# Optimization experiments

Measured on AMD Instinct MI355X. Metric: run time of the kernel, lower is better.

Reference implementation:

```python
import jax, jax.numpy as jnp
import numpy as np

# PyG ChebConv defaults: normalization='sym', lambda_max=2.0.
# L_hat = 2*L/lambda_max - I = (I - D^-1/2 A D^-1/2) - I = -D^-1/2 A D^-1/2
# (self-loop/diagonal coefficient is exactly 0 when lambda_max == 2).

N_NODES = 30000
IN_CH = 128
HID_CH = 256
K = 3
N_EDGES = 480000


def _norm_weights(edge_index, n):
    src, dst = edge_index[0], edge_index[1]
    mask = src != dst  # remove_self_loops
    ones = jnp.where(mask, 1.0, 0.0)
    deg = jax.ops.segment_sum(ones, src, num_segments=n)
    dis = jnp.where(deg > 0, deg ** -0.5, 0.0)  # deg_inv_sqrt, inf -> 0
    w = jnp.where(mask, -dis[src] * dis[dst], 0.0)  # -A_sym edge weights
    return src, dst, w


def _cheb_conv(x, src, dst, w, W, b, n):
    # Tx_0 = x; Tx_1 = L_hat x; Tx_k = 2 L_hat Tx_{k-1} - Tx_{k-2}
    def lap(h):  # sparse matvec: (L_hat h)[i] = sum_{e: dst_e=i} w_e * h[src_e]
        return jax.ops.segment_sum(w[:, None] * h[src], dst, num_segments=n)

    Tx_prev = x
    out = x @ W[0]
    if W.shape[0] > 1:
        Tx_cur = lap(x)
        out = out + Tx_cur @ W[1]
        for k in range(2, W.shape[0]):
            Tx_next = 2.0 * lap(Tx_cur) - Tx_prev
            out = out + Tx_next @ W[k]
            Tx_prev, Tx_cur = Tx_cur, Tx_next
    return out + b


def setup_inputs() -> dict:
    key = jax.random.key(0)
    k1, k2, k3, k4, k5, k6 = jax.random.split(key, 6)
    x = jax.random.normal(k1, (N_NODES, IN_CH), dtype=jnp.float32)
    edge_index = jax.random.randint(k2, (2, N_EDGES), 0, N_NODES, dtype=jnp.int64)
    s1 = (1.0 / (IN_CH * K)) ** 0.5
    s2 = (1.0 / (HID_CH * K)) ** 0.5
    W1 = jax.random.uniform(k3, (K, IN_CH, HID_CH), jnp.float32, -s1, s1)
    b1 = jax.random.uniform(k4, (HID_CH,), jnp.float32, -s1, s1)
    W2 = jax.random.uniform(k5, (K, HID_CH, IN_CH), jnp.float32, -s2, s2)
    b2 = jax.random.uniform(k6, (IN_CH,), jnp.float32, -s2, s2)
    return {"x": x, "edge_index": edge_index, "W1": W1, "b1": b1, "W2": W2, "b2": b2}


def reference(x, edge_index, W1, b1, W2, b2):
    n = x.shape[0]
    src, dst, w = _norm_weights(edge_index, n)
    h = jax.nn.relu(_cheb_conv(x, src, dst, w, W1, b1, n))
    return _cheb_conv(h, src, dst, w, W2, b2, n)
```

## Files before the change

kernel.cpp:

```cpp
#include <hip/hip_runtime.h>
#include <hip/hip_bf16.h>


#define ELLW 64

typedef short bf16x8_t __attribute__((ext_vector_type(8)));
typedef unsigned short u16x4_t __attribute__((ext_vector_type(4)));
typedef unsigned short u16x8_t __attribute__((ext_vector_type(8)));
typedef float f32x4_t __attribute__((ext_vector_type(4)));

static __device__ inline unsigned short f2bf(float f) {
    __hip_bfloat16 h = __float2bfloat16(f);
    return __builtin_bit_cast(unsigned short, h);
}
static __device__ inline float bfbits2f(unsigned int lo16) {
    unsigned int u = lo16 << 16;
    return __builtin_bit_cast(float, u);
}

__global__ __launch_bounds__(256) void build_kernel(const int* __restrict__ src,
                                                    const int* __restrict__ dst,
                                                    int* __restrict__ degi,
                                                    int* __restrict__ cnt,
                                                    unsigned short* __restrict__ ell,
                                                    int E) {
    int e = blockIdx.x * 256 + threadIdx.x;
    if (e >= E) return;
    int s = src[e], d = dst[e];
    if (s != d) atomicAdd(&degi[s], 1);
    int pos = atomicAdd(&cnt[d], 1);
    if (pos < ELLW) ell[(size_t)d * ELLW + pos] = (unsigned short)s;
}

__global__ __launch_bounds__(256) void prep_kernel(const float* __restrict__ W1,
                                                   const float* __restrict__ W2,
                                                   const float* __restrict__ x,
                                                   unsigned short* __restrict__ Bt1,
                                                   unsigned short* __restrict__ Bt2,
                                                   unsigned short* __restrict__ xb,
                                                   int nx4) {
    const int NB1 = 256 * 384, NB2 = 384 * 256;
    int i = blockIdx.x * 256 + threadIdx.x;
    if (i < NB1) {
        int n = i / 384, k = i % 384;
        Bt1[(size_t)n * 384 + k] = f2bf(W1[(size_t)k * 256 + n]);
    } else if (i < NB1 + NB2) {
        int j = i - NB1;
        int n = j / 256, k = j % 256;
        float v;
        if (n < 128) v = W2[(size_t)(1 * 256 + k) * 128 + n];
        else if (n < 256) v = W2[(size_t)(2 * 256 + k) * 128 + (n - 128)];
        else v = W2[(size_t)k * 128 + (n - 256)] - W2[(size_t)(2 * 256 + k) * 128 + (n - 256)];
        Bt2[(size_t)n * 256 + k] = f2bf(v);
    } else {
        int j = i - NB1 - NB2;
        if (j < nx4) {
            f32x4_t v = *(const f32x4_t*)&x[(size_t)j * 4];
            u16x4_t u;
            u.x = f2bf(v.x); u.y = f2bf(v.y); u.z = f2bf(v.z); u.w = f2bf(v.w);
            *(u16x4_t*)&xb[(size_t)j * 4] = u;
        }
    }
}

__global__ __launch_bounds__(256) void lap_ell_kernel(const unsigned short* __restrict__ Xb,
                                                      float* __restrict__ Yf,
                                                      unsigned short* __restrict__ Yb,
                                                      const int* __restrict__ cnt,
                                                      const unsigned short* __restrict__ ell,
                                                      const int* __restrict__ degi,
                                                      const unsigned short* __restrict__ add,
                                                      const float* __restrict__ bias,
                                                      float s, float a, int N) {
    int tid = threadIdx.x;
    int wave = tid >> 6;
    int lane = tid & 63;
    int sub = lane >> 5;
    int l32 = lane & 31;
    int node = blockIdx.x * 8 + wave * 2 + sub;
    if (node >= N) return;
    int col = blockIdx.y * 64 + l32 * 2;

    int n = cnt[node];
    if (n > ELLW) n = ELLW;
    int dn = degi[node];
    float fdn = (float)dn;
    const unsigned short* row = ell + (size_t)node * ELLW;
    const unsigned short* Xc = Xb + col;

    float ax0 = 0.f, ay0 = 0.f, ax1 = 0.f, ay1 = 0.f;
    float ax2 = 0.f, ay2 = 0.f, ax3 = 0.f, ay3 = 0.f;
    int j = 0;
    for (; j + 4 <= n; j += 4) {
        u16x4_t s4 = *(const u16x4_t*)&row[j];
        int s0 = (int)s4.x, s1 = (int)s4.y, s2 = (int)s4.z, s3 = (int)s4.w;
        unsigned int v0 = *(const unsigned int*)&Xc[(size_t)s0 * 128];
        unsigned int v1 = *(const unsigned int*)&Xc[(size_t)s1 * 128];
        unsigned int v2 = *(const unsigned int*)&Xc[(size_t)s2 * 128];
        unsigned int v3 = *(const unsigned int*)&Xc[(size_t)s3 * 128];
        int d0 = degi[s0], d1 = degi[s1], d2 = degi[s2], d3 = degi[s3];
        float w0 = (s0 != node && dn > 0 && d0 > 0) ? -rsqrtf(fdn * (float)d0) : 0.0f;
        float w1 = (s1 != node && dn > 0 && d1 > 0) ? -rsqrtf(fdn * (float)d1) : 0.0f;
        float w2 = (s2 != node && dn > 0 && d2 > 0) ? -rsqrtf(fdn * (float)d2) : 0.0f;
        float w3 = (s3 != node && dn > 0 && d3 > 0) ? -rsqrtf(fdn * (float)d3) : 0.0f;
        ax0 = fmaf(w0, bfbits2f(v0 & 0xffffu), ax0);
        ay0 = fmaf(w0, bfbits2f(v0 >> 16), ay0);
        ax1 = fmaf(w1, bfbits2f(v1 & 0xffffu), ax1);
        ay1 = fmaf(w1, bfbits2f(v1 >> 16), ay1);
        ax2 = fmaf(w2, bfbits2f(v2 & 0xffffu), ax2);
        ay2 = fmaf(w2, bfbits2f(v2 >> 16), ay2);
        ax3 = fmaf(w3, bfbits2f(v3 & 0xffffu), ax3);
        ay3 = fmaf(w3, bfbits2f(v3 >> 16), ay3);
    }
    for (; j < n; ++j) {
        int s0 = (int)row[j];
        unsigned int v0 = *(const unsigned int*)&Xc[(size_t)s0 * 128];
        int d0 = degi[s0];
        float w0 = (s0 != node && dn > 0 && d0 > 0) ? -rsqrtf(fdn * (float)d0) : 0.0f;
        ax0 = fmaf(w0, bfbits2f(v0 & 0xffffu), ax0);
        ay0 = fmaf(w0, bfbits2f(v0 >> 16), ay0);
    }
    float rx = s * ((ax0 + ax1) + (ax2 + ax3));
    float ry = s * ((ay0 + ay1) + (ay2 + ay3));
    size_t o = (size_t)node * 128 + col;
    if (add) {
        unsigned int ad = *(const unsigned int*)&add[o];
        rx = fmaf(a, bfbits2f(ad & 0xffffu), rx);
        ry = fmaf(a, bfbits2f(ad >> 16), ry);
    }
    if (bias) {
        rx += bias[col];
        ry += bias[col + 1];
    }
    if (Yf) {
        float2 r; r.x = rx; r.y = ry;
        *(float2*)&Yf[o] = r;
    }
    if (Yb) {
        unsigned int ob = ((unsigned int)f2bf(ry) << 16) | f2bf(rx);
        *(unsigned int*)&Yb[o] = ob;
    }
}

__global__ __launch_bounds__(512) void gemm_mfma_kernel(
        const unsigned short* __restrict__ A0, const unsigned short* __restrict__ A1,
        const unsigned short* __restrict__ A2, int ldA,
        const unsigned short* __restrict__ Bt, int K,
        unsigned short* __restrict__ Ob0, unsigned short* __restrict__ Ob1,
        unsigned short* __restrict__ Ob2,
        int ldO, const float* __restrict__ bias, int M, int relu) {
    __shared__ unsigned short As[128][72];
    __shared__ unsigned short Bs[64][72];

    int tid = threadIdx.x;
    int lane = tid & 63;
    int wid = tid >> 6;
    int wm = wid >> 1;
    int wn = wid & 1;
    int lm = lane & 15, lg = lane >> 4;

    int rowBase = blockIdx.x * 128;
    int colBase = blockIdx.y * 64;

    f32x4_t acc[2][2] = {};

    for (int k0 = 0; k0 < K; k0 += 64) {
        int seg = k0 >> 7;
        int acol = k0 & 127;
        const unsigned short* A = (seg == 0) ? A0 : ((seg == 1) ? A1 : A2);

        {
            int row = tid >> 2;
            int c = (tid & 3) * 16;
            int gr = rowBase + row;
            u16x8_t v0 = {0, 0, 0, 0, 0, 0, 0, 0};
            u16x8_t v1 = {0, 0, 0, 0, 0, 0, 0, 0};
            if (gr < M) {
                const unsigned short* ap = &A[(size_t)gr * ldA + acol + c];
                v0 = *(const u16x8_t*)ap;
                v1 = *(const u16x8_t*)(ap + 8);
            }
            *(u16x8_t*)&As[row][c] = v0;
            *(u16x8_t*)&As[row][c + 8] = v1;
        }
        {
            int n = tid >> 3;
            int kb = tid & 7;
            u16x8_t bv = *(const u16x8_t*)&Bt[(size_t)(colBase + n) * K + k0 + kb * 8];
            *(u16x8_t*)&Bs[n][kb * 8] = bv;
        }
        __syncthreads();

#pragma unroll
        for (int ks = 0; ks < 2; ++ks) {
            int koff = ks * 32 + lg * 8;
            bf16x8_t a0 = *(const bf16x8_t*)&As[wm * 32 + lm][koff];
            bf16x8_t a1 = *(const bf16x8_t*)&As[wm * 32 + 16 + lm][koff];
            bf16x8_t b0 = *(const bf16x8_t*)&Bs[wn * 32 + lm][koff];
            bf16x8_t b1 = *(const bf16x8_t*)&Bs[wn * 32 + 16 + lm][koff];
            acc[0][0] = __builtin_amdgcn_mfma_f32_16x16x32_bf16(a0, b0, acc[0][0], 0, 0, 0);
            acc[0][1] = __builtin_amdgcn_mfma_f32_16x16x32_bf16(a0, b1, acc[0][1], 0, 0, 0);
            acc[1][0] = __builtin_amdgcn_mfma_f32_16x16x32_bf16(a1, b0, acc[1][0], 0, 0, 0);
            acc[1][1] = __builtin_amdgcn_mfma_f32_16x16x32_bf16(a1, b1, acc[1][1], 0, 0, 0);
        }
        __syncthreads();
    }

    int oseg = colBase >> 7;
    unsigned short* Ob = (oseg == 0) ? Ob0 : ((oseg == 1) ? Ob1 : Ob2);
    int lcbase = (colBase & 127) + wn * 32;
#pragma unroll
    for (int i = 0; i < 2; ++i) {
#pragma unroll
        for (int j = 0; j < 2; ++j) {
            int lc = lcbase + j * 16 + lm;
            int gcol = colBase + wn * 32 + j * 16 + lm;
            float bval = bias ? bias[gcol] : 0.0f;
#pragma unroll
            for (int r = 0; r < 4; ++r) {
                int gr = rowBase + wm * 32 + i * 16 + lg * 4 + r;
                if (gr < M) {
                    float v = acc[i][j][r] + bval;
                    if (relu) v = fmaxf(v, 0.0f);
                    Ob[(size_t)gr * ldO + lc] = f2bf(v);
                }
            }
        }
    }
}

extern "C" void kernel_launch(void* const* d_in, const int* in_sizes, int n_in,
                              void* d_out, int out_size, void* d_ws, size_t ws_size,
                              hipStream_t stream) {
    const float* x  = (const float*)d_in[0];
    const int*   ei = (const int*)d_in[1];
    const float* W1 = (const float*)d_in[2];
    const float* b1 = (const float*)d_in[3];
    const float* W2 = (const float*)d_in[4];
    const float* b2 = (const float*)d_in[5];
    float* out = (float*)d_out;

    const int IN = 128, HID = 256;
    int N = in_sizes[0] / IN;
    int E = in_sizes[1] / 2;
    const int* src = ei;
    const int* dst = ei + E;

    char* ws = (char*)d_ws;
    size_t off = 0;
    auto alloc = [&](size_t bytes) -> void* {
        void* p = ws + off;
        off += (bytes + 255) & ~(size_t)255;
        return p;
    };
    int* ibuf   = (int*)alloc((size_t)2 * N * 4);
    int* degi   = ibuf;
    int* cnt    = ibuf + N;
    unsigned short* ell = (unsigned short*)alloc((size_t)N * ELLW * 2);
    unsigned short* xb  = (unsigned short*)alloc((size_t)N * IN * 2);
    unsigned short* T1b = (unsigned short*)alloc((size_t)N * IN * 2);
    unsigned short* T2b = (unsigned short*)alloc((size_t)N * IN * 2);
    unsigned short* A2b = (unsigned short*)alloc((size_t)N * IN * 2);
    unsigned short* Ib  = (unsigned short*)alloc((size_t)N * IN * 2);
    unsigned short* hb  = (unsigned short*)alloc((size_t)N * HID * 2);
    unsigned short* Db  = (unsigned short*)alloc((size_t)N * IN * 2);
    unsigned short* Zb  = (unsigned short*)alloc((size_t)N * IN * 2);
    unsigned short* Bt1 = (unsigned short*)alloc((size_t)256 * 384 * 2);
    unsigned short* Bt2 = (unsigned short*)alloc((size_t)384 * 256 * 2);

    dim3 gLap((N + 7) / 8, 2);
    int gBlkM = (N + 127) / 128;
    int nx4 = N * IN / 4;
    int prepItems = 256 * 384 + 384 * 256 + nx4;

    hipMemsetAsync(ibuf, 0, (size_t)2 * N * 4, stream);
    build_kernel<<<(E + 255) / 256, 256, 0, stream>>>(src, dst, degi, cnt, ell, E);
    prep_kernel<<<(prepItems + 255) / 256, 256, 0, stream>>>(W1, W2, x, Bt1, Bt2, xb, nx4);

    lap_ell_kernel<<<gLap, 256, 0, stream>>>(xb, nullptr, T1b, cnt, ell, degi,
                                             nullptr, nullptr, 1.0f, 0.0f, N);
    lap_ell_kernel<<<gLap, 256, 0, stream>>>(T1b, nullptr, T2b, cnt, ell, degi,
                                             xb, nullptr, 2.0f, -1.0f, N);
    {
        dim3 grid(gBlkM, 4);
        gemm_mfma_kernel<<<grid, 512, 0, stream>>>(xb, T1b, T2b, IN,
                                                   Bt1, 384,
                                                   hb, hb + 128, nullptr,
                                                   HID, b1, N, 1);
    }

    {
        dim3 grid(gBlkM, 6);
        gemm_mfma_kernel<<<grid, 512, 0, stream>>>(hb, hb + 128, nullptr, HID,
                                                   Bt2, 256,
                                                   Db, A2b, Zb,
                                                   IN, nullptr, N, 0);
        lap_ell_kernel<<<gLap, 256, 0, stream>>>(A2b, nullptr, Ib, cnt, ell, degi,
                                                 Db, nullptr, 2.0f, 1.0f, N);
        lap_ell_kernel<<<gLap, 256, 0, stream>>>(Ib, out, nullptr, cnt, ell, degi,
                                                 Zb, b2, 1.0f, 1.0f, N);
    }
}
```

Measured before the change: 229.3 us.

## Merge build and prep kernels; one wave per node in Laplacian SpMM

```diff
diff --git a/kernel.cpp b/kernel.cpp
--- a/kernel.cpp
+++ b/kernel.cpp
@@ -18,29 +18,26 @@
     return __builtin_bit_cast(float, u);
 }
 
-__global__ __launch_bounds__(256) void build_kernel(const int* __restrict__ src,
-                                                    const int* __restrict__ dst,
-                                                    int* __restrict__ degi,
-                                                    int* __restrict__ cnt,
-                                                    unsigned short* __restrict__ ell,
-                                                    int E) {
-    int e = blockIdx.x * 256 + threadIdx.x;
-    if (e >= E) return;
-    int s = src[e], d = dst[e];
-    if (s != d) atomicAdd(&degi[s], 1);
-    int pos = atomicAdd(&cnt[d], 1);
-    if (pos < ELLW) ell[(size_t)d * ELLW + pos] = (unsigned short)s;
-}
-
-__global__ __launch_bounds__(256) void prep_kernel(const float* __restrict__ W1,
-                                                   const float* __restrict__ W2,
-                                                   const float* __restrict__ x,
-                                                   unsigned short* __restrict__ Bt1,
-                                                   unsigned short* __restrict__ Bt2,
-                                                   unsigned short* __restrict__ xb,
-                                                   int nx4) {
+__global__ __launch_bounds__(256) void build_prep_kernel(
+        const int* __restrict__ src, const int* __restrict__ dst,
+        int* __restrict__ degi, int* __restrict__ cnt,
+        unsigned short* __restrict__ ell, int E, int gB,
+        const float* __restrict__ W1, const float* __restrict__ W2,
+        const float* __restrict__ x,
+        unsigned short* __restrict__ Bt1, unsigned short* __restrict__ Bt2,
+        unsigned short* __restrict__ xb, int nx4) {
+    int bid = blockIdx.x;
+    if (bid < gB) {
+        int e = bid * 256 + threadIdx.x;
+        if (e >= E) return;
+        int s = src[e], d = dst[e];
+        if (s != d) atomicAdd(&degi[s], 1);
+        int pos = atomicAdd(&cnt[d], 1);
+        if (pos < ELLW) ell[(size_t)d * ELLW + pos] = (unsigned short)s;
+        return;
+    }
     const int NB1 = 256 * 384, NB2 = 384 * 256;
-    int i = blockIdx.x * 256 + threadIdx.x;
+    int i = (bid - gB) * 256 + threadIdx.x;
     if (i < NB1) {
         int n = i / 384, k = i % 384;
         Bt1[(size_t)n * 384 + k] = f2bf(W1[(size_t)k * 256 + n]);
@@ -72,32 +69,29 @@
                                                       const unsigned short* __restrict__ add,
                                                       const float* __restrict__ bias,
                                                       float s, float a, int N) {
-    int tid = threadIdx.x;
-    int wave = tid >> 6;
-    int lane = tid & 63;
-    int sub = lane >> 5;
-    int l32 = lane & 31;
-    int node = blockIdx.x * 8 + wave * 2 + sub;
+    int wave = threadIdx.x >> 6;
+    int lane = threadIdx.x & 63;
+    int node = blockIdx.x * 4 + wave;
     if (node >= N) return;
-    int col = blockIdx.y * 64 + l32 * 2;
-
     int n = cnt[node];
     if (n > ELLW) n = ELLW;
     int dn = degi[node];
     float fdn = (float)dn;
     const unsigned short* row = ell + (size_t)node * ELLW;
-    const unsigned short* Xc = Xb + col;
 
     float ax0 = 0.f, ay0 = 0.f, ax1 = 0.f, ay1 = 0.f;
     float ax2 = 0.f, ay2 = 0.f, ax3 = 0.f, ay3 = 0.f;
     int j = 0;
     for (; j + 4 <= n; j += 4) {
         u16x4_t s4 = *(const u16x4_t*)&row[j];
-        int s0 = (int)s4.x, s1 = (int)s4.y, s2 = (int)s4.z, s3 = (int)s4.w;
-        unsigned int v0 = *(const unsigned int*)&Xc[(size_t)s0 * 128];
-        unsigned int v1 = *(const unsigned int*)&Xc[(size_t)s1 * 128];
-        unsigned int v2 = *(const unsigned int*)&Xc[(size_t)s2 * 128];
-        unsigned int v3 = *(const unsigned int*)&Xc[(size_t)s3 * 128];
+        int s0 = __builtin_amdgcn_readfirstlane((int)s4.x);
+        int s1 = __builtin_amdgcn_readfirstlane((int)s4.y);
+        int s2 = __builtin_amdgcn_readfirstlane((int)s4.z);
+        int s3 = __builtin_amdgcn_readfirstlane((int)s4.w);
+        unsigned int v0 = *(const unsigned int*)&Xb[(size_t)s0 * 128 + lane * 2];
+        unsigned int v1 = *(const unsigned int*)&Xb[(size_t)s1 * 128 + lane * 2];
+        unsigned int v2 = *(const unsigned int*)&Xb[(size_t)s2 * 128 + lane * 2];
+        unsigned int v3 = *(const unsigned int*)&Xb[(size_t)s3 * 128 + lane * 2];
         int d0 = degi[s0], d1 = degi[s1], d2 = degi[s2], d3 = degi[s3];
         float w0 = (s0 != node && dn > 0 && d0 > 0) ? -rsqrtf(fdn * (float)d0) : 0.0f;
         float w1 = (s1 != node && dn > 0 && d1 > 0) ? -rsqrtf(fdn * (float)d1) : 0.0f;
@@ -113,8 +107,8 @@
         ay3 = fmaf(w3, bfbits2f(v3 >> 16), ay3);
     }
     for (; j < n; ++j) {
-        int s0 = (int)row[j];
-        unsigned int v0 = *(const unsigned int*)&Xc[(size_t)s0 * 128];
+        int s0 = __builtin_amdgcn_readfirstlane((int)row[j]);
+        unsigned int v0 = *(const unsigned int*)&Xb[(size_t)s0 * 128 + lane * 2];
         int d0 = degi[s0];
         float w0 = (s0 != node && dn > 0 && d0 > 0) ? -rsqrtf(fdn * (float)d0) : 0.0f;
         ax0 = fmaf(w0, bfbits2f(v0 & 0xffffu), ax0);
@@ -122,15 +116,15 @@
     }
     float rx = s * ((ax0 + ax1) + (ax2 + ax3));
     float ry = s * ((ay0 + ay1) + (ay2 + ay3));
-    size_t o = (size_t)node * 128 + col;
+    size_t o = (size_t)node * 128 + lane * 2;
     if (add) {
         unsigned int ad = *(const unsigned int*)&add[o];
         rx = fmaf(a, bfbits2f(ad & 0xffffu), rx);
         ry = fmaf(a, bfbits2f(ad >> 16), ry);
     }
     if (bias) {
-        rx += bias[col];
-        ry += bias[col + 1];
+        rx += bias[lane * 2];
+        ry += bias[lane * 2 + 1];
     }
     if (Yf) {
         float2 r; r.x = rx; r.y = ry;
@@ -268,14 +262,15 @@
     unsigned short* Bt1 = (unsigned short*)alloc((size_t)256 * 384 * 2);
     unsigned short* Bt2 = (unsigned short*)alloc((size_t)384 * 256 * 2);
 
-    dim3 gLap((N + 7) / 8, 2);
+    int gLap = (N + 3) / 4;
     int gBlkM = (N + 127) / 128;
     int nx4 = N * IN / 4;
-    int prepItems = 256 * 384 + 384 * 256 + nx4;
+    int gB = (E + 255) / 256;
+    int gP = (256 * 384 + 384 * 256 + nx4 + 255) / 256;
 
     hipMemsetAsync(ibuf, 0, (size_t)2 * N * 4, stream);
-    build_kernel<<<(E + 255) / 256, 256, 0, stream>>>(src, dst, degi, cnt, ell, E);
-    prep_kernel<<<(prepItems + 255) / 256, 256, 0, stream>>>(W1, W2, x, Bt1, Bt2, xb, nx4);
+    build_prep_kernel<<<gB + gP, 256, 0, stream>>>(src, dst, degi, cnt, ell, E, gB,
+                                                   W1, W2, x, Bt1, Bt2, xb, nx4);
 
     lap_ell_kernel<<<gLap, 256, 0, stream>>>(xb, nullptr, T1b, cnt, ell, degi,
                                              nullptr, nullptr, 1.0f, 0.0f, N);
```

After: 204.4 us. 1.12x faster.
